# Performance work log

Hardware: AMD Instinct MI355X
Metric: run time of the kernel (lower is better)

## Reference

```python
import jax, jax.numpy as jnp
import numpy as np

K = 3
PAD = 1
STRIDE = 1
DIL = 1


def _conv(x, w, b):
    # standard 3x3 conv, NCHW / OIHW
    y = jax.lax.conv_general_dilated(
        x, w, (STRIDE, STRIDE), [(PAD, PAD), (PAD, PAD)],
        rhs_dilation=(DIL, DIL),
        dimension_numbers=('NCHW', 'OIHW', 'NCHW'))
    return y + b[None, :, None, None]


def _deform_conv2d(x, offset, mask, weight, bias):
    # x: [B,C,H,W]; offset: [B,2*KK,Ho,Wo] (y,x interleaved per kernel tap);
    # mask: [B,KK,Ho,Wo]; weight: [Co,C,K,K]; bias: [Co]
    B, C, H, W = x.shape
    KK = K * K
    Ho, Wo = offset.shape[2], offset.shape[3]

    off = offset.reshape(B, KK, 2, Ho, Wo)
    dy, dx = off[:, :, 0], off[:, :, 1]          # [B,KK,Ho,Wo]

    ky, kx = jnp.meshgrid(jnp.arange(K), jnp.arange(K), indexing='ij')
    ky = ky.reshape(KK).astype(x.dtype)
    kx = kx.reshape(KK).astype(x.dtype)
    hs = (jnp.arange(Ho) * STRIDE - PAD).astype(x.dtype)
    ws = (jnp.arange(Wo) * STRIDE - PAD).astype(x.dtype)
    base_y = hs[None, :, None] + (ky * DIL)[:, None, None]   # [KK,Ho,1]
    base_x = ws[None, None, :] + (kx * DIL)[:, None, None]   # [KK,1,Wo]

    py = base_y[None] + dy                        # [B,KK,Ho,Wo] sample rows
    px = base_x[None] + dx                        # sample cols

    y0 = jnp.floor(py)
    x0 = jnp.floor(px)
    ly = py - y0                                  # bilinear fractional weights
    lx = px - x0
    y0i = y0.astype(jnp.int32)
    x0i = x0.astype(jnp.int32)

    flat = x.reshape(B, C, H * W)

    def gather(iy, ix):
        # zero-padded gather at integer locations -> [B,C,KK,Ho,Wo]
        valid = (iy >= 0) & (iy < H) & (ix >= 0) & (ix < W)
        iyc = jnp.clip(iy, 0, H - 1)
        ixc = jnp.clip(ix, 0, W - 1)
        idx = (iyc * W + ixc).reshape(B, 1, KK * Ho * Wo)
        g = jnp.take_along_axis(flat, jnp.broadcast_to(idx, (B, C, KK * Ho * Wo)), axis=2)
        g = g.reshape(B, C, KK, Ho, Wo)
        return g * valid[:, None].astype(x.dtype)

    val = (gather(y0i, x0i) * ((1 - ly) * (1 - lx))[:, None]
           + gather(y0i, x0i + 1) * ((1 - ly) * lx)[:, None]
           + gather(y0i + 1, x0i) * (ly * (1 - lx))[:, None]
           + gather(y0i + 1, x0i + 1) * (ly * lx)[:, None])

    val = val * mask[:, None]                     # DCNv2 modulation

    wr = weight.reshape(weight.shape[0], C, KK)   # [Co,C,KK]
    out = jnp.einsum('bckhw,ock->bohw', val, wr)
    return out + bias[None, :, None, None]


def setup_inputs() -> dict:
    key = jax.random.key(0)
    ks = jax.random.split(key, 7)
    B, C, Co, H, W = 4, 128, 256, 96, 96
    KK = K * K
    x = jax.random.normal(ks[0], (B, C, H, W), dtype=jnp.float32)
    weight = jax.random.normal(ks[1], (Co, C, K, K), dtype=jnp.float32) * 0.03
    bias = jax.random.normal(ks[2], (Co,), dtype=jnp.float32) * 0.01
    offset_w = jax.random.normal(ks[3], (2 * KK, C, K, K), dtype=jnp.float32) * 0.01
    offset_b = jax.random.normal(ks[4], (2 * KK,), dtype=jnp.float32) * 0.01
    mod_w = jax.random.normal(ks[5], (KK, C, K, K), dtype=jnp.float32) * 0.01
    mod_b = jnp.ones((KK,), dtype=jnp.float32)
    return {'x': x, 'weight': weight, 'bias': bias,
            'offset_w': offset_w, 'offset_b': offset_b,
            'mod_w': mod_w, 'mod_b': mod_b}


def reference(x, weight, bias, offset_w, offset_b, mod_w, mod_b):
    offset = _conv(x, offset_w, offset_b)
    mask = jax.nn.sigmoid(_conv(x, mod_w, mod_b))
    return _deform_conv2d(x, offset, mask, weight, bias)
```

## Files before the change

### kernel.cpp

```cpp
#include <hip/hip_runtime.h>
#include <math.h>

#define HH 96
#define WW 96
#define HW 9216
#define CIN 128
#define COUT 256

typedef _Float16 f16;
typedef _Float16 f16x2 __attribute__((ext_vector_type(2)));
typedef _Float16 f16x8 __attribute__((ext_vector_type(8)));
typedef __attribute__((ext_vector_type(4))) float f32x4;

static __device__ __forceinline__ unsigned short f2h(float f) {
  union { f16 h; unsigned short u; } v; v.h = (f16)f; return v.u;
}

__global__ __launch_bounds__(256) void k_prep(const float* __restrict__ x,
                                              const float* __restrict__ offw,
                                              const float* __restrict__ modw,
                                              const float* __restrict__ wgt,
                                              unsigned short* __restrict__ xTh,
                                              unsigned short* __restrict__ wAbF,
                                              unsigned short* __restrict__ wTtF) {
  __shared__ float tile[32][129];
  int bid = blockIdx.x;
  int t = threadIdx.x;
  if (bid < 1152) {
    int wseg = bid % 3, h = (bid / 3) % 96, b = bid / 288;
    int wl = t & 31, cg = t >> 5;
    const float* xp = x + ((size_t)(b * 128 + cg) * 96 + h) * 96 + wseg * 32 + wl;
#pragma unroll
    for (int i = 0; i < 16; ++i)
      tile[wl][cg + 8 * i] = xp[(size_t)8 * i * HW];
    __syncthreads();
    int cl = t & 127, wg = t >> 7;
    unsigned short* op = xTh + (((size_t)(b * 96 + h) * 96) + wseg * 32) * 128 + cl;
#pragma unroll
    for (int i = 0; i < 16; ++i)
      op[(size_t)(wg + 2 * i) * 128] = f2h(tile[wg + 2 * i][cl]);
  } else if (bid < 1296) {
    int i = (bid - 1152) * 256 + t;
    if (i < 9 * 2 * 4 * 512) {
      int j = i & 7;
      int l = (i >> 3) & 63;
      int ks = (i >> 9) & 3;
      int ng = i >> 11;
      int kpos = ng >> 1, n16 = ng & 1;
      int n = n16 * 16 + (l & 15);
      int c = ks * 32 + (l >> 4) * 8 + j;
      float v = 0.f;
      if (n < 18) v = offw[n * 1152 + c * 9 + kpos];
      else if (n < 27) v = modw[(n - 18) * 1152 + c * 9 + kpos];
      wAbF[i] = f2h(v);
    }
  } else {
    int i = (bid - 1296) * 256 + t;
    if (i < 9 * 16 * 4 * 512) {
      int j = i & 7;
      int l = (i >> 3) & 63;
      int ks = (i >> 9) & 3;
      int ng = i >> 11;
      int kpos = ng >> 4, n16 = ng & 15;
      int n = n16 * 16 + (l & 15);
      int c = ks * 32 + (l >> 4) * 8 + j;
      wTtF[i] = f2h(wgt[n * 1152 + c * 9 + kpos]);
    }
  }
}

__global__ __launch_bounds__(256) void k_main(const unsigned short* __restrict__ xTh,
                                              const unsigned short* __restrict__ wAbF,
                                              const unsigned short* __restrict__ wTtF,
                                              const float* __restrict__ offb,
                                              const float* __restrict__ modb,
                                              const float* __restrict__ bias,
                                              float* __restrict__ out) {
  __shared__ __align__(16) unsigned short Ab[32 * 72];
  __shared__ float om_lds[27 * 33];
  __shared__ float ez[4 * 1040];

  int t = threadIdx.x;
  int l = t & 63, w = t >> 6;
  int lm = l & 15, lq = l >> 4;
  int raw = blockIdx.x;
  int bid = (raw & 7) * 144 + (raw >> 3);
  int pix0 = bid * 32;
  int b = pix0 / HW;
  int posim0 = pix0 % HW;
  int ibase = b * HW;

  {
    int mh = w & 1, n16o = w >> 1;
    int prow = pix0 + mh * 16 + lm;
    int pimo = prow % HW;
    int hoo = pimo / 96, woo = pimo % 96;
    f32x4 acco = (f32x4){0.f, 0.f, 0.f, 0.f};
    const f16x8 zv = {0, 0, 0, 0, 0, 0, 0, 0};
#pragma unroll 1
    for (int kpos = 0; kpos < 9; ++kpos) {
      int dyr = kpos / 3 - 1, dxr = kpos % 3 - 1;
      bool valid = ((unsigned)(hoo + dyr) < 96u) && ((unsigned)(woo + dxr) < 96u);
      int srow = valid ? (prow + dyr * 96 + dxr) : prow;
      const unsigned short* ap = xTh + (size_t)srow * 128 + lq * 8;
      const unsigned short* bp = wAbF + (size_t)((kpos * 2 + n16o) * 4) * 512 + l * 8;
#pragma unroll
      for (int ks = 0; ks < 4; ++ks) {
        f16x8 af = valid ? *(const f16x8*)(ap + ks * 32) : zv;
        f16x8 bf = *(const f16x8*)(bp + (size_t)ks * 512);
        acco = __builtin_amdgcn_mfma_f32_16x16x32_f16(af, bf, acco, 0, 0, 0);
      }
    }
    int n = n16o * 16 + lm;
    if (n < 27) {
      float bv = (n < 18) ? offb[n] : modb[n - 18];
#pragma unroll
      for (int r = 0; r < 4; ++r) {
        float v = acco[r] + bv;
        if (n >= 18) v = 1.f / (1.f + expf(-v));
        om_lds[n * 33 + mh * 16 + lq * 4 + r] = v;
      }
    }
  }
  __syncthreads();

  int px = t & 31;
  int oct = t >> 5;
  int pim = (pix0 + px) % HW;
  int ho = pim / 96, wo = pim % 96;

  f32x4 acc[2][4];
#pragma unroll
  for (int i = 0; i < 2; ++i)
#pragma unroll
    for (int j = 0; j < 4; ++j)
      acc[i][j] = (f32x4){0.f, 0.f, 0.f, 0.f};

  for (int kpos = 0; kpos < 9; ++kpos) {
    float dy = om_lds[(2 * kpos) * 33 + px];
    float dx = om_lds[(2 * kpos + 1) * 33 + px];
    float mk = om_lds[(18 + kpos) * 33 + px];
    float py = (float)(ho - 1 + kpos / 3) + dy;
    float pxf = (float)(wo - 1 + kpos % 3) + dx;
    float fy = floorf(py), fx = floorf(pxf);
    int y0 = (int)fy, x0 = (int)fx;
    float ly = py - fy, lx = pxf - fx;
    float w00 = (1.f - ly) * (1.f - lx), w01 = (1.f - ly) * lx;
    float w10 = ly * (1.f - lx),         w11 = ly * lx;
    bool vy0 = (unsigned)y0 < 96u, vy1 = (unsigned)(y0 + 1) < 96u;
    bool vx0 = (unsigned)x0 < 96u, vx1 = (unsigned)(x0 + 1) < 96u;
    w00 = (vy0 && vx0) ? w00 * mk : 0.f;
    w01 = (vy0 && vx1) ? w01 * mk : 0.f;
    w10 = (vy1 && vx0) ? w10 * mk : 0.f;
    w11 = (vy1 && vx1) ? w11 * mk : 0.f;
    int y0c = min(max(y0, 0), 95), y1c = min(max(y0 + 1, 0), 95);
    int x0c = min(max(x0, 0), 95), x1c = min(max(x0 + 1, 0), 95);
    int o00 = (ibase + y0c * 96 + x0c) * 128;
    int o01 = (ibase + y0c * 96 + x1c) * 128;
    int o10 = (ibase + y1c * 96 + x0c) * 128;
    int o11 = (ibase + y1c * 96 + x1c) * 128;
    f16 h00 = (f16)w00, h01 = (f16)w01, h10 = (f16)w10, h11 = (f16)w11;
    f16x2 wp00 = (f16x2){h00, h00}, wp01 = (f16x2){h01, h01};
    f16x2 wp10 = (f16x2){h10, h10}, wp11 = (f16x2){h11, h11};

#pragma unroll
    for (int half = 0; half < 2; ++half) {
      int cc = half * 64 + oct * 8;
      __syncthreads();
      {
        union { uint4 u; f16x2 h[4]; } a0, a1, a2, a3;
        a0.u = *(const uint4*)(xTh + o00 + cc);
        a1.u = *(const uint4*)(xTh + o01 + cc);
        a2.u = *(const uint4*)(xTh + o10 + cc);
        a3.u = *(const uint4*)(xTh + o11 + cc);
        union { f16x8 v; f16x2 h[4]; } r;
#pragma unroll
        for (int j = 0; j < 4; ++j)
          r.h[j] = a0.h[j] * wp00 + a1.h[j] * wp01 + a2.h[j] * wp10 + a3.h[j] * wp11;
        *(f16x8*)(Ab + px * 72 + oct * 8) = r.v;
      }
      __syncthreads();
#pragma unroll
      for (int ks = 0; ks < 2; ++ks) {
        f16x8 af[2], bfv[4];
#pragma unroll
        for (int mt = 0; mt < 2; ++mt)
          af[mt] = *(const f16x8*)(Ab + (mt * 16 + lm) * 72 + ks * 32 + lq * 8);
        const unsigned short* bp =
            wTtF + (size_t)((kpos * 16 + w * 4) * 4 + 2 * half + ks) * 512 + l * 8;
#pragma unroll
        for (int nt = 0; nt < 4; ++nt)
          bfv[nt] = *(const f16x8*)(bp + (size_t)nt * 4 * 512);
#pragma unroll
        for (int mt = 0; mt < 2; ++mt)
#pragma unroll
          for (int nt = 0; nt < 4; ++nt)
            acc[mt][nt] = __builtin_amdgcn_mfma_f32_16x16x32_f16(af[mt], bfv[nt], acc[mt][nt], 0, 0, 0);
      }
    }
  }

  float bias_v[4];
#pragma unroll
  for (int nt = 0; nt < 4; ++nt) bias_v[nt] = bias[w * 64 + nt * 16 + lm];
  float* z = ez + w * 1040;
#pragma unroll
  for (int mt = 0; mt < 2; ++mt) {
    __syncthreads();
#pragma unroll
    for (int nt = 0; nt < 4; ++nt)
#pragma unroll
      for (int r = 0; r < 4; ++r)
        z[(lq * 4 + r) * 65 + nt * 16 + lm] = acc[mt][nt][r] + bias_v[nt];
    __syncthreads();
    int pxr = l & 15;
    int nb = l >> 4;
#pragma unroll
    for (int s = 0; s < 16; ++s) {
      int n = nb + 4 * s;
      out[((size_t)(b * COUT + w * 64 + n)) * HW + posim0 + mt * 16 + pxr] = z[pxr * 65 + n];
    }
  }
}

extern "C" void kernel_launch(void* const* d_in, const int* in_sizes, int n_in,
                              void* d_out, int out_size, void* d_ws, size_t ws_size,
                              hipStream_t stream) {
  const float* x      = (const float*)d_in[0];
  const float* weight = (const float*)d_in[1];
  const float* bias   = (const float*)d_in[2];
  const float* offw   = (const float*)d_in[3];
  const float* offb   = (const float*)d_in[4];
  const float* modw   = (const float*)d_in[5];
  const float* modb   = (const float*)d_in[6];
  float* out = (float*)d_out;
  float* ws = (float*)d_ws;

  unsigned short* xTh  = (unsigned short*)ws;
  unsigned short* wTtF = (unsigned short*)(ws + 2359296);
  unsigned short* wAbF = (unsigned short*)(ws + 2359296 + 147456);

  k_prep<<<2448, 256, 0, stream>>>(x, offw, modw, weight, xTh, wAbF, wTtF);
  k_main<<<1152, 256, 0, stream>>>(xTh, wAbF, wTtF, offb, modb, bias, out);
}
```

Measured before the change: 175.8 us.

## Double pixel tile per block to 64 to reuse weight fragments across more rows

Each block now handles 64 output pixels instead of 32, so every B-fragment of the deformable-conv weight loaded from global memory feeds four M-tiles instead of two. This halves the weight traffic per pixel. The offset/mask conv is restructured so each wave handles 16 pixels and both N-tiles, and the epilogue is rewritten to stage per-16-channel slabs and store 64 contiguous pixels per row. The cost is twice the accumulator registers and fewer blocks (576), which can lower occupancy and leave fewer blocks to spread across CUs.

After: 185.1 us. 1.05x slower.

```diff
diff --git a/kernel.cpp b/kernel.cpp
--- a/kernel.cpp
+++ b/kernel.cpp
@@ -76,26 +76,28 @@
                                               const float* __restrict__ modb,
                                               const float* __restrict__ bias,
                                               float* __restrict__ out) {
-  __shared__ __align__(16) unsigned short Ab[32 * 72];
-  __shared__ float om_lds[27 * 33];
-  __shared__ float ez[4 * 1040];
+  __shared__ __align__(16) unsigned short Ab[64 * 72];
+  __shared__ __align__(16) float ezs[4 * 1088];
+  __shared__ float om_lds[27 * 65];
 
   int t = threadIdx.x;
-  int l = t & 63, w = t >> 6;
+  int l = t & 63;
+  int w = t >> 6;
   int lm = l & 15, lq = l >> 4;
   int raw = blockIdx.x;
-  int bid = (raw & 7) * 144 + (raw >> 3);
-  int pix0 = bid * 32;
+  int bid = (raw & 7) * 72 + (raw >> 3);
+  int pix0 = bid * 64;
   int b = pix0 / HW;
   int posim0 = pix0 % HW;
   int ibase = b * HW;
 
   {
-    int mh = w & 1, n16o = w >> 1;
-    int prow = pix0 + mh * 16 + lm;
+    int prow = pix0 + w * 16 + lm;
     int pimo = prow % HW;
     int hoo = pimo / 96, woo = pimo % 96;
-    f32x4 acco = (f32x4){0.f, 0.f, 0.f, 0.f};
+    f32x4 acco[2];
+    acco[0] = (f32x4){0.f, 0.f, 0.f, 0.f};
+    acco[1] = (f32x4){0.f, 0.f, 0.f, 0.f};
     const f16x8 zv = {0, 0, 0, 0, 0, 0, 0, 0};
 #pragma unroll 1
     for (int kpos = 0; kpos < 9; ++kpos) {
@@ -103,43 +105,48 @@
       bool valid = ((unsigned)(hoo + dyr) < 96u) && ((unsigned)(woo + dxr) < 96u);
       int srow = valid ? (prow + dyr * 96 + dxr) : prow;
       const unsigned short* ap = xTh + (size_t)srow * 128 + lq * 8;
-      const unsigned short* bp = wAbF + (size_t)((kpos * 2 + n16o) * 4) * 512 + l * 8;
+      const unsigned short* bp = wAbF + (size_t)(kpos * 8) * 512 + l * 8;
 #pragma unroll
       for (int ks = 0; ks < 4; ++ks) {
         f16x8 af = valid ? *(const f16x8*)(ap + ks * 32) : zv;
-        f16x8 bf = *(const f16x8*)(bp + (size_t)ks * 512);
-        acco = __builtin_amdgcn_mfma_f32_16x16x32_f16(af, bf, acco, 0, 0, 0);
-      }
-    }
-    int n = n16o * 16 + lm;
-    if (n < 27) {
-      float bv = (n < 18) ? offb[n] : modb[n - 18];
-#pragma unroll
-      for (int r = 0; r < 4; ++r) {
-        float v = acco[r] + bv;
-        if (n >= 18) v = 1.f / (1.f + expf(-v));
-        om_lds[n * 33 + mh * 16 + lq * 4 + r] = v;
+        f16x8 bf0 = *(const f16x8*)(bp + (size_t)ks * 512);
+        f16x8 bf1 = *(const f16x8*)(bp + (size_t)(4 + ks) * 512);
+        acco[0] = __builtin_amdgcn_mfma_f32_16x16x32_f16(af, bf0, acco[0], 0, 0, 0);
+        acco[1] = __builtin_amdgcn_mfma_f32_16x16x32_f16(af, bf1, acco[1], 0, 0, 0);
+      }
+    }
+#pragma unroll
+    for (int nt = 0; nt < 2; ++nt) {
+      int n = nt * 16 + lm;
+      if (n < 27) {
+        float bv = (n < 18) ? offb[n] : modb[n - 18];
+#pragma unroll
+        for (int r = 0; r < 4; ++r) {
+          float v = acco[nt][r] + bv;
+          if (n >= 18) v = 1.f / (1.f + expf(-v));
+          om_lds[n * 65 + w * 16 + lq * 4 + r] = v;
+        }
       }
     }
   }
   __syncthreads();
 
-  int px = t & 31;
-  int oct = t >> 5;
-  int pim = (pix0 + px) % HW;
-  int ho = pim / 96, wo = pim % 96;
-
-  f32x4 acc[2][4];
-#pragma unroll
-  for (int i = 0; i < 2; ++i)
+  int px = t & 63;
+  int basegrp = t >> 6;
+  int pos = pix0 + px;
+  int ho = (pos % HW) / 96, wo = pos % 96;
+
+  f32x4 acc[4][4];
+#pragma unroll
+  for (int i = 0; i < 4; ++i)
 #pragma unroll
     for (int j = 0; j < 4; ++j)
       acc[i][j] = (f32x4){0.f, 0.f, 0.f, 0.f};
 
   for (int kpos = 0; kpos < 9; ++kpos) {
-    float dy = om_lds[(2 * kpos) * 33 + px];
-    float dx = om_lds[(2 * kpos + 1) * 33 + px];
-    float mk = om_lds[(18 + kpos) * 33 + px];
+    float dy = om_lds[(2 * kpos) * 65 + px];
+    float dx = om_lds[(2 * kpos + 1) * 65 + px];
+    float mk = om_lds[(18 + kpos) * 65 + px];
     float py = (float)(ho - 1 + kpos / 3) + dy;
     float pxf = (float)(wo - 1 + kpos % 3) + dx;
     float fy = floorf(py), fx = floorf(pxf);
@@ -165,9 +172,12 @@
 
 #pragma unroll
     for (int half = 0; half < 2; ++half) {
-      int cc = half * 64 + oct * 8;
+      int c0 = half * 64;
       __syncthreads();
-      {
+#pragma unroll
+      for (int item = 0; item < 2; ++item) {
+        int oct = basegrp + 4 * item;
+        int cc = c0 + oct * 8;
         union { uint4 u; f16x2 h[4]; } a0, a1, a2, a3;
         a0.u = *(const uint4*)(xTh + o00 + cc);
         a1.u = *(const uint4*)(xTh + o01 + cc);
@@ -182,9 +192,9 @@
       __syncthreads();
 #pragma unroll
       for (int ks = 0; ks < 2; ++ks) {
-        f16x8 af[2], bfv[4];
-#pragma unroll
-        for (int mt = 0; mt < 2; ++mt)
+        f16x8 af[4], bfv[4];
+#pragma unroll
+        for (int mt = 0; mt < 4; ++mt)
           af[mt] = *(const f16x8*)(Ab + (mt * 16 + lm) * 72 + ks * 32 + lq * 8);
         const unsigned short* bp =
             wTtF + (size_t)((kpos * 16 + w * 4) * 4 + 2 * half + ks) * 512 + l * 8;
@@ -192,7 +202,7 @@
         for (int nt = 0; nt < 4; ++nt)
           bfv[nt] = *(const f16x8*)(bp + (size_t)nt * 4 * 512);
 #pragma unroll
-        for (int mt = 0; mt < 2; ++mt)
+        for (int mt = 0; mt < 4; ++mt)
 #pragma unroll
           for (int nt = 0; nt < 4; ++nt)
             acc[mt][nt] = __builtin_amdgcn_mfma_f32_16x16x32_f16(af[mt], bfv[nt], acc[mt][nt], 0, 0, 0);
@@ -203,23 +213,20 @@
   float bias_v[4];
 #pragma unroll
   for (int nt = 0; nt < 4; ++nt) bias_v[nt] = bias[w * 64 + nt * 16 + lm];
-  float* z = ez + w * 1040;
-#pragma unroll
-  for (int mt = 0; mt < 2; ++mt) {
+  float* ez = ezs + w * 1088;
+#pragma unroll
+  for (int nt = 0; nt < 4; ++nt) {
     __syncthreads();
 #pragma unroll
-    for (int nt = 0; nt < 4; ++nt)
+    for (int mt = 0; mt < 4; ++mt)
 #pragma unroll
       for (int r = 0; r < 4; ++r)
-        z[(lq * 4 + r) * 65 + nt * 16 + lm] = acc[mt][nt][r] + bias_v[nt];
+        ez[(mt * 16 + lq * 4 + r) * 17 + lm] = acc[mt][nt][r] + bias_v[nt];
     __syncthreads();
-    int pxr = l & 15;
-    int nb = l >> 4;
-#pragma unroll
-    for (int s = 0; s < 16; ++s) {
-      int n = nb + 4 * s;
-      out[((size_t)(b * COUT + w * 64 + n)) * HW + posim0 + mt * 16 + pxr] = z[pxr * 65 + n];
-    }
+    float* ob = out + ((size_t)(b * COUT + w * 64 + nt * 16)) * HW + posim0;
+#pragma unroll
+    for (int j = 0; j < 16; ++j)
+      ob[(size_t)j * HW + l] = ez[l * 17 + j];
   }
 }
 
@@ -241,5 +248,5 @@
   unsigned short* wAbF = (unsigned short*)(ws + 2359296 + 147456);
 
   k_prep<<<2448, 256, 0, stream>>>(x, offw, modw, weight, xTh, wAbF, wTtF);
-  k_main<<<1152, 256, 0, stream>>>(xTh, wAbF, wTtF, offb, modb, bias, out);
-}
+  k_main<<<576, 256, 0, stream>>>(xTh, wAbF, wTtF, offb, modb, bias, out);
+}
```

## Stage all 128 channels per tap in one LDS tile with hoisted gathers

Applied to the files above, without the earlier changes.

The bilinear-gather A tile now holds all 128 input channels for a kernel tap instead of two 64-channel halves. Thread mapping changes so 8 threads cover one pixel's 128 channels, each doing two 16-byte gathers per corner. All global gathers are issued before the barrier, and there are two barriers per tap instead of four. This lets the gathers overlap the previous tap's MFMAs and cuts synchronisation, at the cost of more registers (eight uint4 per thread) and twice the LDS for the A tile.

Result: faster. 149.6 us (-14.9%).

```diff
diff --git a/kernel.cpp b/kernel.cpp
--- a/kernel.cpp
+++ b/kernel.cpp
@@ -76,7 +76,7 @@
                                               const float* __restrict__ modb,
                                               const float* __restrict__ bias,
                                               float* __restrict__ out) {
-  __shared__ __align__(16) unsigned short Ab[32 * 72];
+  __shared__ __align__(16) unsigned short Ab[32 * 136];
   __shared__ float om_lds[27 * 33];
   __shared__ float ez[4 * 1040];
 
@@ -124,10 +124,10 @@
   }
   __syncthreads();
 
-  int px = t & 31;
-  int oct = t >> 5;
-  int pim = (pix0 + px) % HW;
-  int ho = pim / 96, wo = pim % 96;
+  int pxo = t >> 3;
+  int sc8 = t & 7;
+  int pimS = (pix0 + pxo) % HW;
+  int hoS = pimS / 96, woS = pimS % 96;
 
   f32x4 acc[2][4];
 #pragma unroll
@@ -137,11 +137,11 @@
       acc[i][j] = (f32x4){0.f, 0.f, 0.f, 0.f};
 
   for (int kpos = 0; kpos < 9; ++kpos) {
-    float dy = om_lds[(2 * kpos) * 33 + px];
-    float dx = om_lds[(2 * kpos + 1) * 33 + px];
-    float mk = om_lds[(18 + kpos) * 33 + px];
-    float py = (float)(ho - 1 + kpos / 3) + dy;
-    float pxf = (float)(wo - 1 + kpos % 3) + dx;
+    float dy = om_lds[(2 * kpos) * 33 + pxo];
+    float dx = om_lds[(2 * kpos + 1) * 33 + pxo];
+    float mk = om_lds[(18 + kpos) * 33 + pxo];
+    float py = (float)(hoS - 1 + kpos / 3) + dy;
+    float pxf = (float)(woS - 1 + kpos % 3) + dx;
     float fy = floorf(py), fx = floorf(pxf);
     int y0 = (int)fy, x0 = (int)fx;
     float ly = py - fy, lx = pxf - fx;
@@ -155,48 +155,52 @@
     w11 = (vy1 && vx1) ? w11 * mk : 0.f;
     int y0c = min(max(y0, 0), 95), y1c = min(max(y0 + 1, 0), 95);
     int x0c = min(max(x0, 0), 95), x1c = min(max(x0 + 1, 0), 95);
-    int o00 = (ibase + y0c * 96 + x0c) * 128;
-    int o01 = (ibase + y0c * 96 + x1c) * 128;
-    int o10 = (ibase + y1c * 96 + x0c) * 128;
-    int o11 = (ibase + y1c * 96 + x1c) * 128;
+    int ofs[4];
+    ofs[0] = (ibase + y0c * 96 + x0c) * 128;
+    ofs[1] = (ibase + y0c * 96 + x1c) * 128;
+    ofs[2] = (ibase + y1c * 96 + x0c) * 128;
+    ofs[3] = (ibase + y1c * 96 + x1c) * 128;
     f16 h00 = (f16)w00, h01 = (f16)w01, h10 = (f16)w10, h11 = (f16)w11;
-    f16x2 wp00 = (f16x2){h00, h00}, wp01 = (f16x2){h01, h01};
-    f16x2 wp10 = (f16x2){h10, h10}, wp11 = (f16x2){h11, h11};
-
-#pragma unroll
-    for (int half = 0; half < 2; ++half) {
-      int cc = half * 64 + oct * 8;
-      __syncthreads();
-      {
-        union { uint4 u; f16x2 h[4]; } a0, a1, a2, a3;
-        a0.u = *(const uint4*)(xTh + o00 + cc);
-        a1.u = *(const uint4*)(xTh + o01 + cc);
-        a2.u = *(const uint4*)(xTh + o10 + cc);
-        a3.u = *(const uint4*)(xTh + o11 + cc);
-        union { f16x8 v; f16x2 h[4]; } r;
-#pragma unroll
-        for (int j = 0; j < 4; ++j)
-          r.h[j] = a0.h[j] * wp00 + a1.h[j] * wp01 + a2.h[j] * wp10 + a3.h[j] * wp11;
-        *(f16x8*)(Ab + px * 72 + oct * 8) = r.v;
-      }
-      __syncthreads();
-#pragma unroll
-      for (int ks = 0; ks < 2; ++ks) {
-        f16x8 af[2], bfv[4];
-#pragma unroll
-        for (int mt = 0; mt < 2; ++mt)
-          af[mt] = *(const f16x8*)(Ab + (mt * 16 + lm) * 72 + ks * 32 + lq * 8);
-        const unsigned short* bp =
-            wTtF + (size_t)((kpos * 16 + w * 4) * 4 + 2 * half + ks) * 512 + l * 8;
+    f16x2 wp[4];
+    wp[0] = (f16x2){h00, h00}; wp[1] = (f16x2){h01, h01};
+    wp[2] = (f16x2){h10, h10}; wp[3] = (f16x2){h11, h11};
+
+    uint4 q[4][2];
+#pragma unroll
+    for (int c = 0; c < 4; ++c)
+#pragma unroll
+      for (int it = 0; it < 2; ++it)
+        q[c][it] = *(const uint4*)(xTh + ofs[c] + (sc8 + 8 * it) * 8);
+
+    __syncthreads();
+#pragma unroll
+    for (int it = 0; it < 2; ++it) {
+      union { uint4 u; f16x2 h[4]; } a0, a1, a2, a3;
+      a0.u = q[0][it]; a1.u = q[1][it]; a2.u = q[2][it]; a3.u = q[3][it];
+      union { f16x8 v; f16x2 h[4]; } r;
+#pragma unroll
+      for (int j = 0; j < 4; ++j)
+        r.h[j] = a0.h[j] * wp[0] + a1.h[j] * wp[1] + a2.h[j] * wp[2] + a3.h[j] * wp[3];
+      *(f16x8*)(Ab + pxo * 136 + (sc8 + 8 * it) * 8) = r.v;
+    }
+    __syncthreads();
+
+#pragma unroll
+    for (int ks = 0; ks < 4; ++ks) {
+      f16x8 af[2], bfv[4];
+#pragma unroll
+      for (int mt = 0; mt < 2; ++mt)
+        af[mt] = *(const f16x8*)(Ab + (mt * 16 + lm) * 136 + ks * 32 + lq * 8);
+      const unsigned short* bp =
+          wTtF + (size_t)((kpos * 16 + w * 4) * 4 + ks) * 512 + l * 8;
+#pragma unroll
+      for (int nt = 0; nt < 4; ++nt)
+        bfv[nt] = *(const f16x8*)(bp + (size_t)nt * 4 * 512);
+#pragma unroll
+      for (int mt = 0; mt < 2; ++mt)
 #pragma unroll
         for (int nt = 0; nt < 4; ++nt)
-          bfv[nt] = *(const f16x8*)(bp + (size_t)nt * 4 * 512);
-#pragma unroll
-        for (int mt = 0; mt < 2; ++mt)
-#pragma unroll
-          for (int nt = 0; nt < 4; ++nt)
-            acc[mt][nt] = __builtin_amdgcn_mfma_f32_16x16x32_f16(af[mt], bfv[nt], acc[mt][nt], 0, 0, 0);
-      }
+          acc[mt][nt] = __builtin_amdgcn_mfma_f32_16x16x32_f16(af[mt], bfv[nt], acc[mt][nt], 0, 0, 0);
     }
   }
 
```
